# Performance work log

Hardware: AMD Instinct MI355X
Metric: run time of the kernel (lower is better)

Reference implementation:

```python
import jax, jax.numpy as jnp
import numpy as np

HIDDEN = 768
MLP_RATIO = 4
HID_F = HIDDEN * MLP_RATIO          # 3072
NUM_EXPERTS = 6
PART = 192                           # part_features
SHARED = HIDDEN - PART               # 576
B, S = 32, 1024


def setup_inputs() -> dict:
    key = jax.random.key(0)
    ks = jax.random.split(key, 8)
    hidden_state = jax.random.normal(ks[0], (B, S, HIDDEN), dtype=jnp.float32)
    indices = jax.random.randint(ks[1], (B,), 0, NUM_EXPERTS, dtype=jnp.int64)
    sc1 = 1.0 / np.sqrt(HIDDEN)
    sc2 = 1.0 / np.sqrt(HID_F)
    W1 = jax.random.normal(ks[2], (HIDDEN, HID_F), dtype=jnp.float32) * sc1
    b1 = jax.random.normal(ks[3], (HID_F,), dtype=jnp.float32) * sc1
    W2 = jax.random.normal(ks[4], (HID_F, SHARED), dtype=jnp.float32) * sc2
    b2 = jax.random.normal(ks[5], (SHARED,), dtype=jnp.float32) * sc2
    We = jax.random.normal(ks[6], (NUM_EXPERTS, HID_F, PART), dtype=jnp.float32) * sc2
    be = jax.random.normal(ks[7], (NUM_EXPERTS, PART), dtype=jnp.float32) * sc2
    return {"hidden_state": hidden_state, "indices": indices,
            "W1": W1, "b1": b1, "W2": W2, "b2": b2, "We": We, "be": be}


def reference(hidden_state, indices, W1, b1, W2, b2, We, be):
    # fc1 + exact GELU (torch ACT2FN['gelu'])
    h = jnp.einsum('bsd,df->bsf', hidden_state, W1) + b1          # [B,S,HID_F]
    h = jax.nn.gelu(h, approximate=False)
    # shared branch
    shared = jnp.einsum('bsf,fo->bso', h, W2) + b2                # [B,S,SHARED]
    # expert branch: indices select exactly one expert per batch element,
    # so the masked sum over all experts equals gathering the routed expert.
    Wsel = We[indices]                                            # [B,HID_F,PART]
    bsel = be[indices]                                            # [B,PART]
    expert = jnp.einsum('bsf,bfp->bsp', h, Wsel) + bsel[:, None, :]
    return jnp.concatenate([shared, expert], axis=-1)             # [B,S,HIDDEN]
```

## Files before the change

kernel.cpp:

```cpp
#include <hip/hip_runtime.h>
#include <hip/hip_bf16.h>
#include <cstdint>
#include <cstddef>

#define HIDDEN   768
#define HID_F    3072
#define PART     192
#define SHARED_F 576
#define NEXP     6
#define BATCH    32
#define SEQ      1024
#define M_TOK    (BATCH * SEQ)

typedef __bf16 bf16;
typedef __attribute__((ext_vector_type(8))) __bf16 bf16x8;
typedef __attribute__((ext_vector_type(4))) __bf16 bf16x4;
typedef __attribute__((ext_vector_type(4))) float  f32x4;

__device__ __forceinline__ void gl2lds16(const void* g, void* l) {
    __builtin_amdgcn_global_load_lds(
        (const __attribute__((address_space(1))) void*)g,
        (__attribute__((address_space(3))) void*)l,
        16, 0, 0);
}

__device__ __forceinline__ f32x4 mfma16(bf16x8 a, bf16x8 b, f32x4 c) {
    return __builtin_amdgcn_mfma_f32_16x16x32_bf16(a, b, c, 0, 0, 0);
}

#define CFENCE() asm volatile("" ::: "memory")
__device__ __forceinline__ void barrier_raw() {
    CFENCE();
    __builtin_amdgcn_s_barrier();
    CFENCE();
}

__device__ __forceinline__ float gelu_fast(float x) {
    float xs = x * 0.70710678118654752f;
    float ax = __builtin_fabsf(xs);
    float t  = __builtin_amdgcn_rcpf(1.0f + 0.3275911f * ax);
    float p  = t * (0.254829592f +
               t * (-0.284496736f +
               t * (1.421413741f +
               t * (-1.453152027f +
               t * 1.061405429f))));
    float e  = __expf(-xs * xs);
    float er = 1.0f - p * e;
    er = (xs < 0.0f) ? -er : er;
    return 0.5f * x * (1.0f + er);
}

__global__ __launch_bounds__(256) void cvt_f32_bf16(
        const float4* __restrict__ src, bf16x4* __restrict__ dst, int n4) {
    int i      = blockIdx.x * 256 + threadIdx.x;
    int stride = gridDim.x * 256;
    for (; i < n4; i += stride) {
        float4 v = src[i];
        bf16x4 o = { (__bf16)v.x, (__bf16)v.y, (__bf16)v.z, (__bf16)v.w };
        dst[i] = o;
    }
}

__global__ __launch_bounds__(256) void transpose_cvt(
        const float* __restrict__ src, bf16* __restrict__ dst, int K, int N) {
    __shared__ float t[32][33];
    const int n0 = blockIdx.x * 32, k0 = blockIdx.y * 32;
    const int tx = threadIdx.x & 31, ty = threadIdx.x >> 5;
#pragma unroll
    for (int p = 0; p < 4; ++p) {
        int r = ty + p * 8;
        t[r][tx] = src[(size_t)(k0 + r) * N + n0 + tx];
    }
    __syncthreads();
#pragma unroll
    for (int p = 0; p < 4; ++p) {
        int rn = ty + p * 8;
        dst[(size_t)(n0 + rn) * K + k0 + tx] = (bf16)t[tx][rn];
    }
}

__global__ __launch_bounds__(256) void build_wcat(
        const float* __restrict__ W2, const float* __restrict__ We,
        bf16* __restrict__ Wcat) {
    __shared__ float t[32][33];
    const int e  = blockIdx.z;
    const int n0 = blockIdx.x * 32;
    const int k0 = blockIdx.y * 32;
    const int tx = threadIdx.x & 31, ty = threadIdx.x >> 5;
    const float* src;
    int ld, c;
    if (n0 < SHARED_F) { src = W2; ld = SHARED_F; c = n0 + tx; }
    else { src = We + (size_t)e * HID_F * PART; ld = PART; c = n0 + tx - SHARED_F; }
#pragma unroll
    for (int p = 0; p < 4; ++p) {
        int r = ty + p * 8;
        t[r][tx] = src[(size_t)(k0 + r) * ld + c];
    }
    __syncthreads();
    bf16* dst = Wcat + (size_t)e * HIDDEN * HID_F;
#pragma unroll
    for (int p = 0; p < 4; ++p) {
        int rn = ty + p * 8;
        dst[(size_t)(n0 + rn) * HID_F + k0 + tx] = (bf16)t[tx][rn];
    }
}


#define STAGE_A(kt, hm, bb) do {                                          \
    const bf16* g_ = gA + (size_t)((hm) * 128) * LDA + (kt) * 64;         \
    bf16* l_ = lA + ((bb) * 2 + (hm)) * 8192;                             \
    gl2lds16(g_, l_);                                                     \
    gl2lds16(g_ + (size_t)64 * LDA, l_ + 4096);                           \
} while (0)

#define STAGE_B(kt, hm, bb) do {                                          \
    const bf16* g_ = gB + (size_t)((hm) * 128) * LDB + (kt) * 64;         \
    bf16* l_ = lB + ((bb) * 2 + (hm)) * 8192;                             \
    gl2lds16(g_, l_);                                                     \
    gl2lds16(g_ + (size_t)64 * LDB, l_ + 4096);                           \
} while (0)

#define LOAD_A(qm, bb) do {                                               \
    const bf16* ab_ = fA + ((bb) * 2 + (qm)) * 8192;                      \
    _Pragma("unroll")                                                     \
    for (int mi = 0; mi < 4; ++mi) {                                      \
        af[mi][0] = *(const bf16x8*)(ab_ + mi * 1024 + pca0);             \
        af[mi][1] = *(const bf16x8*)(ab_ + mi * 1024 + pca1);             \
    }                                                                     \
} while (0)

#define LOAD_B(qn, bb) do {                                               \
    const bf16* bb_ = fB + ((bb) * 2 + (qn)) * 8192;                      \
    _Pragma("unroll")                                                     \
    for (int nj = 0; nj < 2; ++nj) {                                      \
        bfr[nj][0] = *(const bf16x8*)(bb_ + nj * 1024 + pcb0);            \
        bfr[nj][1] = *(const bf16x8*)(bb_ + nj * 1024 + pcb1);            \
    }                                                                     \
} while (0)

#define MFMA_CLUSTER(qm, qn) do {                                         \
    __builtin_amdgcn_s_setprio(1);                                        \
    _Pragma("unroll")                                                     \
    for (int mi = 0; mi < 4; ++mi)                                        \
        _Pragma("unroll")                                                 \
        for (int nj = 0; nj < 2; ++nj) {                                  \
            acc[(qm)*4+mi][(qn)*2+nj] =                                   \
                mfma16(af[mi][0], bfr[nj][0], acc[(qm)*4+mi][(qn)*2+nj]); \
            acc[(qm)*4+mi][(qn)*2+nj] =                                   \
                mfma16(af[mi][1], bfr[nj][1], acc[(qm)*4+mi][(qn)*2+nj]); \
        }                                                                 \
    __builtin_amdgcn_s_setprio(0);                                        \
} while (0)

template<bool IS_FC1>
__global__ __launch_bounds__(512, 2) void fc_8ph(
        const bf16*  __restrict__ A,
        const bf16*  __restrict__ Bmat,
        const float* __restrict__ bias1,
        const float* __restrict__ bias2,
        const int*   __restrict__ idx,
        void*        __restrict__ Outv) {
    constexpr int LDA     = IS_FC1 ? HIDDEN : HID_F;
    constexpr int LDB     = LDA;
    constexpr int NT      = LDA / 64;
    constexpr int NTILE_N = IS_FC1 ? (HID_F / 256) : (HIDDEN / 256);
    constexpr int LDOUT   = IS_FC1 ? HID_F : HIDDEN;

    __shared__ alignas(16) bf16 Abuf[2 * 2 * 128 * 64];
    __shared__ alignas(16) bf16 Bbuf[2 * 2 * 128 * 64];

    const int tid  = threadIdx.x;
    const int wave = tid >> 6, lane = tid & 63;
    const int wm = wave >> 2, wn = wave & 3;
    const int lrow = lane & 15, lk8 = (lane >> 4) & 3;

    const int L   = blockIdx.x;
    const int xcd = L & 7;
    const int j   = L >> 3;
    const int jm  = j / NTILE_N;
    const int mt  = xcd * 16 + jm;
    const int nt  = j - jm * NTILE_N;
    const int m0  = mt * 256;
    const int n0  = nt * 256;

    const bf16* Bt;
    int e = 0;
    if constexpr (IS_FC1) {
        Bt = Bmat;
    } else {
        e = idx[mt >> 2];
        e = e < 0 ? 0 : (e > NEXP - 1 ? NEXP - 1 : e);
        Bt = Bmat + (size_t)e * HIDDEN * HID_F;
    }

    const int srow = tid >> 3;
    const int lch  = (tid & 7) ^ (srow & 7);
    const bf16* gA = A  + (size_t)(m0 + srow) * LDA + lch * 8;
    const bf16* gB = Bt + (size_t)(n0 + srow) * LDB + lch * 8;
    bf16* lA = Abuf + wave * 512;
    bf16* lB = Bbuf + wave * 512;

    const int rA = wm * 64 + lrow;
    const int rB = wn * 32 + lrow;
    const int pca0 = ((0 + lk8) ^ (rA & 7)) * 8;
    const int pca1 = ((4 + lk8) ^ (rA & 7)) * 8;
    const int pcb0 = ((0 + lk8) ^ (rB & 7)) * 8;
    const int pcb1 = ((4 + lk8) ^ (rB & 7)) * 8;
    const bf16* fA = Abuf + rA * 64;
    const bf16* fB = Bbuf + rB * 64;

    f32x4 acc[8][4] = {};
    bf16x8 af[4][2], bfr[2][2];

    STAGE_A(0, 0, 0); STAGE_B(0, 0, 0); STAGE_B(0, 1, 0); STAGE_A(0, 1, 0);
    STAGE_A(1, 0, 1); STAGE_B(1, 0, 1);
    asm volatile("s_waitcnt vmcnt(8)" ::: "memory");
    barrier_raw();

#pragma unroll 1
    for (int t = 0; t < NT; ++t) {
        const int b   = t & 1;
        const int bo  = b ^ 1;
        const int tb1 = (t + 1 < NT) ? t + 1 : t - 1;
        const int ta2 = (t + 2 < NT) ? t + 2 : t;

        LOAD_A(0, b);
        LOAD_B(0, b);
        STAGE_B(tb1, 1, bo);
        barrier_raw();
        MFMA_CLUSTER(0, 0);
        asm volatile("s_waitcnt vmcnt(6)" ::: "memory");
        barrier_raw();

        LOAD_B(1, b);
        STAGE_A(tb1, 1, bo);
        barrier_raw();
        MFMA_CLUSTER(0, 1);
        barrier_raw();

        LOAD_A(1, b);
        LOAD_B(0, b);
        STAGE_A(ta2, 0, b);
        barrier_raw();
        MFMA_CLUSTER(1, 0);
        barrier_raw();

        LOAD_B(1, b);
        STAGE_B(ta2, 0, b);
        barrier_raw();
        MFMA_CLUSTER(1, 1);
        asm volatile("s_waitcnt vmcnt(8)" ::: "memory");
        barrier_raw();
    }

    float bv[4];
#pragma unroll
    for (int nj2 = 0; nj2 < 4; ++nj2) {
        const int col = n0 + (nj2 >> 1) * 128 + wn * 32 + (nj2 & 1) * 16 + lrow;
        if constexpr (IS_FC1) {
            bv[nj2] = bias1[col];
        } else {
            bv[nj2] = (col < SHARED_F) ? bias1[col]
                                       : bias2[e * PART + col - SHARED_F];
        }
    }
#pragma unroll
    for (int mi2 = 0; mi2 < 8; ++mi2) {
        const int row0 = m0 + (mi2 >> 2) * 128 + wm * 64 + (mi2 & 3) * 16 + lk8 * 4;
#pragma unroll
        for (int nj2 = 0; nj2 < 4; ++nj2) {
            const int col = n0 + (nj2 >> 1) * 128 + wn * 32 + (nj2 & 1) * 16 + lrow;
            if constexpr (IS_FC1) {
                bf16* o = (bf16*)Outv;
#pragma unroll
                for (int r = 0; r < 4; ++r)
                    o[(size_t)(row0 + r) * LDOUT + col] =
                        (bf16)gelu_fast(acc[mi2][nj2][r] + bv[nj2]);
            } else {
                float* o = (float*)Outv;
#pragma unroll
                for (int r = 0; r < 4; ++r)
                    o[(size_t)(row0 + r) * LDOUT + col] =
                        acc[mi2][nj2][r] + bv[nj2];
            }
        }
    }
}

extern "C" void kernel_launch(void* const* d_in, const int* in_sizes, int n_in,
                              void* d_out, int out_size, void* d_ws, size_t ws_size,
                              hipStream_t stream) {
    const float* hidden = (const float*)d_in[0];
    const int*   idx    = (const int*)d_in[1];
    const float* W1     = (const float*)d_in[2];
    const float* b1     = (const float*)d_in[3];
    const float* W2     = (const float*)d_in[4];
    const float* b2     = (const float*)d_in[5];
    const float* We     = (const float*)d_in[6];
    const float* be     = (const float*)d_in[7];
    float* out = (float*)d_out;

    char* ws = (char*)d_ws;
    bf16* hb   = (bf16*)(ws);
    bf16* h    = (bf16*)(ws + 50331648);
    bf16* W1t  = (bf16*)(ws + 251658240);
    bf16* Wcat = (bf16*)(ws + 256376832);

    cvt_f32_bf16<<<4096, 256, 0, stream>>>(
        (const float4*)hidden, (bf16x4*)hb, (M_TOK * HIDDEN) / 4);
    transpose_cvt<<<dim3(HID_F / 32, HIDDEN / 32), 256, 0, stream>>>(
        W1, W1t, HIDDEN, HID_F);
    build_wcat<<<dim3(HIDDEN / 32, HID_F / 32, NEXP), 256, 0, stream>>>(
        W2, We, Wcat);

    fc_8ph<true><<<(M_TOK / 256) * (HID_F / 256), 512, 0, stream>>>(
        hb, W1t, b1, nullptr, nullptr, h);

    fc_8ph<false><<<(M_TOK / 256) * (HIDDEN / 256), 512, 0, stream>>>(
        h, Wcat, b2, be, idx, out);
}
```

Measured before the change: 642.5 us.

## Double-buffer register fragments and cut per-tile barriers in GEMM main loop

Restructures the K-loop of the 8-phase GEMM so the A and B register fragments are double-buffered (afr0/afr1, bfr0/bfr1). Each tile now has two barriers instead of eight, and the next tile's first fragments are read from LDS before the last MFMA cluster of the current tile. The loop is unrolled by two so the buffer indices are compile-time constants. The aim is to overlap LDS reads with MFMAs and cut synchronisation stalls, at the cost of more VGPRs and more delicate vmcnt and LDS hazard ordering, which could risk races or lower occupancy.

```diff
diff --git a/kernel.cpp b/kernel.cpp
--- a/kernel.cpp
+++ b/kernel.cpp
@@ -120,36 +120,61 @@
     gl2lds16(g_ + (size_t)64 * LDB, l_ + 4096);                           \
 } while (0)
 
-#define LOAD_A(qm, bb) do {                                               \
+#define RD_A(dst, qm, bb) do {                                            \
     const bf16* ab_ = fA + ((bb) * 2 + (qm)) * 8192;                      \
     _Pragma("unroll")                                                     \
     for (int mi = 0; mi < 4; ++mi) {                                      \
-        af[mi][0] = *(const bf16x8*)(ab_ + mi * 1024 + pca0);             \
-        af[mi][1] = *(const bf16x8*)(ab_ + mi * 1024 + pca1);             \
+        dst[mi][0] = *(const bf16x8*)(ab_ + mi * 1024 + pca0);            \
+        dst[mi][1] = *(const bf16x8*)(ab_ + mi * 1024 + pca1);            \
     }                                                                     \
 } while (0)
 
-#define LOAD_B(qn, bb) do {                                               \
+#define RD_B(dst, qn, bb) do {                                            \
     const bf16* bb_ = fB + ((bb) * 2 + (qn)) * 8192;                      \
     _Pragma("unroll")                                                     \
     for (int nj = 0; nj < 2; ++nj) {                                      \
-        bfr[nj][0] = *(const bf16x8*)(bb_ + nj * 1024 + pcb0);            \
-        bfr[nj][1] = *(const bf16x8*)(bb_ + nj * 1024 + pcb1);            \
+        dst[nj][0] = *(const bf16x8*)(bb_ + nj * 1024 + pcb0);            \
+        dst[nj][1] = *(const bf16x8*)(bb_ + nj * 1024 + pcb1);            \
     }                                                                     \
 } while (0)
 
-#define MFMA_CLUSTER(qm, qn) do {                                         \
+#define MFMA16(A_, B_, qm, qn) do {                                       \
     __builtin_amdgcn_s_setprio(1);                                        \
     _Pragma("unroll")                                                     \
     for (int mi = 0; mi < 4; ++mi)                                        \
         _Pragma("unroll")                                                 \
         for (int nj = 0; nj < 2; ++nj) {                                  \
             acc[(qm)*4+mi][(qn)*2+nj] =                                   \
-                mfma16(af[mi][0], bfr[nj][0], acc[(qm)*4+mi][(qn)*2+nj]); \
+                mfma16(A_[mi][0], B_[nj][0], acc[(qm)*4+mi][(qn)*2+nj]);  \
             acc[(qm)*4+mi][(qn)*2+nj] =                                   \
-                mfma16(af[mi][1], bfr[nj][1], acc[(qm)*4+mi][(qn)*2+nj]); \
+                mfma16(A_[mi][1], B_[nj][1], acc[(qm)*4+mi][(qn)*2+nj]);  \
         }                                                                 \
     __builtin_amdgcn_s_setprio(0);                                        \
+} while (0)
+
+#define TILE(t, b, bo) do {                                               \
+    const int tb1_ = ((t) + 1 < NT) ? (t) + 1 : (t) - 1;                  \
+    const int ta2_ = ((t) + 2 < NT) ? (t) + 2 : (t);                      \
+     \
+    asm volatile("s_waitcnt vmcnt(4)" ::: "memory");                      \
+    barrier_raw();                                                        \
+    RD_B(bfr1, 1, b);                                                     \
+    STAGE_B(tb1_, 1, bo);                                                 \
+    MFMA16(afr0, bfr0, 0, 0);                                             \
+     \
+    RD_A(afr1, 1, b);                                                     \
+    STAGE_A(tb1_, 1, bo);                                                 \
+    MFMA16(afr0, bfr1, 0, 1);                                             \
+     \
+    STAGE_A(ta2_, 0, b);                                                  \
+    MFMA16(afr1, bfr0, 1, 0);                                             \
+     \
+    asm volatile("s_waitcnt vmcnt(6)" ::: "memory");                      \
+    barrier_raw();                                                        \
+    RD_A(afr0, 0, bo);                                                    \
+    RD_B(bfr0, 0, bo);                                                    \
+    STAGE_B(ta2_, 0, b);                                                  \
+    MFMA16(afr1, bfr1, 1, 1);                                             \
 } while (0)
 
 template<bool IS_FC1>
@@ -210,47 +235,20 @@
     const bf16* fB = Bbuf + rB * 64;
 
     f32x4 acc[8][4] = {};
-    bf16x8 af[4][2], bfr[2][2];
-
-    STAGE_A(0, 0, 0); STAGE_B(0, 0, 0); STAGE_B(0, 1, 0); STAGE_A(0, 1, 0);
+    bf16x8 afr0[4][2], afr1[4][2], bfr0[2][2], bfr1[2][2];
+
+    STAGE_A(0, 0, 0); STAGE_B(0, 0, 0);
+    STAGE_B(0, 1, 0); STAGE_A(0, 1, 0);
     STAGE_A(1, 0, 1); STAGE_B(1, 0, 1);
     asm volatile("s_waitcnt vmcnt(8)" ::: "memory");
     barrier_raw();
+    RD_A(afr0, 0, 0);
+    RD_B(bfr0, 0, 0);
 
 #pragma unroll 1
-    for (int t = 0; t < NT; ++t) {
-        const int b   = t & 1;
-        const int bo  = b ^ 1;
-        const int tb1 = (t + 1 < NT) ? t + 1 : t - 1;
-        const int ta2 = (t + 2 < NT) ? t + 2 : t;
-
-        LOAD_A(0, b);
-        LOAD_B(0, b);
-        STAGE_B(tb1, 1, bo);
-        barrier_raw();
-        MFMA_CLUSTER(0, 0);
-        asm volatile("s_waitcnt vmcnt(6)" ::: "memory");
-        barrier_raw();
-
-        LOAD_B(1, b);
-        STAGE_A(tb1, 1, bo);
-        barrier_raw();
-        MFMA_CLUSTER(0, 1);
-        barrier_raw();
-
-        LOAD_A(1, b);
-        LOAD_B(0, b);
-        STAGE_A(ta2, 0, b);
-        barrier_raw();
-        MFMA_CLUSTER(1, 0);
-        barrier_raw();
-
-        LOAD_B(1, b);
-        STAGE_B(ta2, 0, b);
-        barrier_raw();
-        MFMA_CLUSTER(1, 1);
-        asm volatile("s_waitcnt vmcnt(8)" ::: "memory");
-        barrier_raw();
+    for (int t = 0; t < NT; t += 2) {
+        TILE(t,     0, 1);
+        TILE(t + 1, 1, 0);
     }
 
     float bv[4];
```

Result: faster. 555.6 us (-13.5%).
